# Optimization experiments

Hardware: AMD Instinct MI355X
Metric: run time of the kernel (lower is better)

The kernel has to match this reference:

```python
import jax, jax.numpy as jnp
import numpy as np

DIM = 512
H = 8          # num_heads
C = 64         # dim_head
HID = H * C    # 512
NMEM = H       # num_mem_kv = num_heads


def _rmsnorm_seq(x, w):
    # F.normalize(x, dim=2) * w * sqrt(dim)
    n = jnp.sqrt(jnp.sum(x * x, axis=2, keepdims=True))
    return x / jnp.maximum(n, 1e-12) * w * jnp.asarray(DIM ** 0.5, x.dtype)


def setup_inputs() -> dict:
    key = jax.random.key(0)
    ks = jax.random.split(key, 7)
    b, n = 4, 4096
    x = jax.random.normal(ks[0], (b, n, DIM), dtype=jnp.float32)
    norm_w = jnp.ones((1, 1, DIM), dtype=jnp.float32)
    w_qkv = jax.random.normal(ks[1], (DIM, 3 * HID), dtype=jnp.float32) / np.sqrt(DIM)
    mem_kv = jax.random.normal(ks[2], (2, H, C, NMEM), dtype=jnp.float32)
    w_out = jax.random.normal(ks[3], (HID, DIM), dtype=jnp.float32) / np.sqrt(HID)
    b_out = jax.random.normal(ks[4], (DIM,), dtype=jnp.float32) * 0.01
    out_norm_w = jnp.ones((1, 1, DIM), dtype=jnp.float32)
    return {"x": x, "norm_w": norm_w, "w_qkv": w_qkv, "mem_kv": mem_kv,
            "w_out": w_out, "b_out": b_out, "out_norm_w": out_norm_w}


def reference(x, norm_w, w_qkv, mem_kv, w_out, b_out, out_norm_w):
    b, n, _ = x.shape
    scale = jnp.asarray(C ** -0.5, x.dtype)
    xn = _rmsnorm_seq(x, norm_w)
    qkv = xn @ w_qkv                                   # [b, n, 3*HID]
    q, k, v = jnp.split(qkv, 3, axis=2)
    # b n (h c) -> b h c n
    def to_heads(t):
        return t.reshape(b, n, H, C).transpose(0, 2, 3, 1)
    q, k, v = map(to_heads, (q, k, v))                 # [b, H, C, n]
    mk = jnp.broadcast_to(mem_kv[0], (b, H, C, NMEM))
    mv = jnp.broadcast_to(mem_kv[1], (b, H, C, NMEM))
    k = jnp.concatenate([mk, k], axis=-1)              # [b, H, C, n+NMEM]
    v = jnp.concatenate([mv, v], axis=-1)
    q = jax.nn.softmax(q, axis=-2) * scale             # softmax over feature dim c
    k = jax.nn.softmax(k, axis=-1)                     # softmax over token dim n
    context = jnp.einsum('bhdn,bhen->bhde', k, v)      # [b, H, C, C]
    out = jnp.einsum('bhde,bhdn->bhen', context, q)    # [b, H, C, n]
    out = out.transpose(0, 3, 1, 2).reshape(b, n, HID)  # b h c n -> b n (h c)
    out = out @ w_out + b_out
    return _rmsnorm_seq(out, out_norm_w)
```

## Files before the change

kernel.cpp:

```cpp
#include <hip/hip_runtime.h>
#include <hip/hip_bf16.h>


typedef __attribute__((ext_vector_type(8))) __bf16 bf16x8;
typedef __attribute__((ext_vector_type(4))) __bf16 bf16x4;
typedef __attribute__((ext_vector_type(2))) __bf16 bf16x2;
typedef __attribute__((ext_vector_type(4))) float f32x4;

#define SQRT_DIM 22.627416997969522f

__device__ __forceinline__ void gload_lds16(const void* g, void* l) {
  __builtin_amdgcn_global_load_lds((__attribute__((address_space(1))) void*)g,
                                   (__attribute__((address_space(3))) void*)l, 16, 0, 0);
}

__global__ __launch_bounds__(256) void pre_k(const float* __restrict__ x,
                                             const float* __restrict__ nw,
                                             __bf16* __restrict__ xn,
                                             const float* __restrict__ wqkv,
                                             __bf16* __restrict__ WqkvT) {
  __shared__ float tbuf[64][65];
  const int bid = blockIdx.x;
  const int tid = threadIdx.x;
  if (bid < 4096) {
    const int row = bid * 4 + (tid >> 6);
    const int lane = tid & 63;
    const float4* xr = (const float4*)(x + (size_t)row * 512);
    float4 v0 = xr[lane], v1 = xr[lane + 64];
    float s = v0.x * v0.x + v0.y * v0.y + v0.z * v0.z + v0.w * v0.w +
              v1.x * v1.x + v1.y * v1.y + v1.z * v1.z + v1.w * v1.w;
#pragma unroll
    for (int m = 1; m < 64; m <<= 1) s += __shfl_xor(s, m);
    const float sc = SQRT_DIM / fmaxf(sqrtf(s), 1e-12f);
    const float4* wr4 = (const float4*)nw;
    float4 w0 = wr4[lane], w1 = wr4[lane + 64];
    __bf16* o = xn + (size_t)row * 512;
    bf16x4 a, b2;
    a[0] = (__bf16)(v0.x * sc * w0.x); a[1] = (__bf16)(v0.y * sc * w0.y);
    a[2] = (__bf16)(v0.z * sc * w0.z); a[3] = (__bf16)(v0.w * sc * w0.w);
    b2[0] = (__bf16)(v1.x * sc * w1.x); b2[1] = (__bf16)(v1.y * sc * w1.y);
    b2[2] = (__bf16)(v1.z * sc * w1.z); b2[3] = (__bf16)(v1.w * sc * w1.w);
    *(bf16x4*)(o + lane * 4) = a;
    *(bf16x4*)(o + 256 + lane * 4) = b2;
  } else {
    const int t = bid - 4096;
    const int bx = t % 24, by = t / 24;
    const int n0 = bx * 64, k0 = by * 64;
    const int r = tid >> 4, c4 = (tid & 15) * 4;
#pragma unroll
    for (int p = 0; p < 4; ++p) {
      float4 v = *(const float4*)(wqkv + (size_t)(k0 + p * 16 + r) * 1536 + n0 + c4);
      tbuf[p * 16 + r][c4 + 0] = v.x;
      tbuf[p * 16 + r][c4 + 1] = v.y;
      tbuf[p * 16 + r][c4 + 2] = v.z;
      tbuf[p * 16 + r][c4 + 3] = v.w;
    }
    __syncthreads();
    const int base = (n0 < 512) ? n0
                     : (n0 < 1024 ? 512 + ((n0 - 512) >> 6) * 128
                                  : 512 + ((n0 - 1024) >> 6) * 128 + 64);
#pragma unroll
    for (int p = 0; p < 4; ++p) {
      int c = p * 256 + tid;
      int rn = c >> 4, cc = (c & 15) * 4;
      bf16x4 o;
#pragma unroll
      for (int j = 0; j < 4; ++j) o[j] = (__bf16)tbuf[cc + j][rn];
      *(bf16x4*)(WqkvT + (size_t)(base + rn) * 512 + k0 + cc) = o;
    }
  }
}

__global__ __launch_bounds__(512) void gemm1_k(const __bf16* __restrict__ A,
                                               const __bf16* __restrict__ BT,
                                               __bf16* __restrict__ QS,
                                               __bf16* __restrict__ pctx,
                                               float* __restrict__ pden) {
  __shared__ __align__(16) char smem[65536];
  const int K = 512;
  const int NT = 8;
  const int NX = 12;
  const int tid = threadIdx.x;
  const int lane = tid & 63;
  const int wave = tid >> 6;
  const int wr = (wave >> 1) * 32;
  const int wc = (wave & 1) * 64;
  const int l15 = lane & 15, lg = lane >> 4;
  const int cpx = gridDim.x >> 3;
  const int fid = blockIdx.x;
  const int tile = (fid & 7) * cpx + (fid >> 3);
  const int my = tile / NX;
  const int m0 = my * 128;
  const int n0 = (tile - my * NX) * 128;
  const int sw0 = lg ^ (l15 & 7);
  const int sw1 = (4 + lg) ^ (l15 & 7);

  f32x4 acc[2][4] = {};

  auto stage = [&](int buf, int k0) {
#pragma unroll
    for (int it = 0; it < 2; ++it) {
      int flat = it * 512 + tid;
      int row = flat >> 3;
      int cb = ((flat & 7) ^ (row & 7)) * 16;
      gload_lds16((const char*)(A + (size_t)(m0 + row) * K + k0) + cb,
                  smem + buf * 16384 + flat * 16);
    }
#pragma unroll
    for (int it = 0; it < 2; ++it) {
      int flat = it * 512 + tid;
      int row = flat >> 3;
      int cb = ((flat & 7) ^ (row & 7)) * 16;
      gload_lds16((const char*)(BT + (size_t)(n0 + row) * K + k0) + cb,
                  smem + 32768 + buf * 16384 + flat * 16);
    }
  };

  stage(0, 0);
  stage(1, 64);
  asm volatile("s_waitcnt vmcnt(4)" ::: "memory");
  __builtin_amdgcn_s_barrier();

  for (int kt = 0; kt < NT; ++kt) {
    const int cur = kt & 1;
    const __bf16* Asb = (const __bf16*)(smem + cur * 16384);
    const __bf16* Bsb = (const __bf16*)(smem + 32768 + cur * 16384);
    bf16x8 a0[2], b0[4], a1[2], b1[4];
#pragma unroll
    for (int i = 0; i < 2; ++i) {
      a0[i] = *(const bf16x8*)(&Asb[(wr + i * 16 + l15) * 64 + sw0 * 8]);
      a1[i] = *(const bf16x8*)(&Asb[(wr + i * 16 + l15) * 64 + sw1 * 8]);
    }
#pragma unroll
    for (int i = 0; i < 4; ++i) {
      b0[i] = *(const bf16x8*)(&Bsb[(wc + i * 16 + l15) * 64 + sw0 * 8]);
      b1[i] = *(const bf16x8*)(&Bsb[(wc + i * 16 + l15) * 64 + sw1 * 8]);
    }
    asm volatile("s_waitcnt lgkmcnt(0)" ::: "memory");
    __builtin_amdgcn_sched_barrier(0);
    __builtin_amdgcn_s_barrier();
    if (kt + 2 < NT) stage(cur, (kt + 2) * 64);
    __builtin_amdgcn_s_setprio(1);
#pragma unroll
    for (int mi = 0; mi < 2; ++mi)
#pragma unroll
      for (int ni = 0; ni < 4; ++ni)
        acc[mi][ni] = __builtin_amdgcn_mfma_f32_16x16x32_bf16(a0[mi], b0[ni],
                                                              acc[mi][ni], 0, 0, 0);
    __builtin_amdgcn_s_setprio(0);
    __builtin_amdgcn_s_setprio(1);
#pragma unroll
    for (int mi = 0; mi < 2; ++mi)
#pragma unroll
      for (int ni = 0; ni < 4; ++ni)
        acc[mi][ni] = __builtin_amdgcn_mfma_f32_16x16x32_bf16(a1[mi], b1[ni],
                                                              acc[mi][ni], 0, 0, 0);
    __builtin_amdgcn_s_setprio(0);
    if (kt < NT - 1) {
      if (kt + 2 < NT)
        asm volatile("s_waitcnt vmcnt(4)" ::: "memory");
      else
        asm volatile("s_waitcnt vmcnt(0)" ::: "memory");
      __builtin_amdgcn_s_barrier();
    }
  }

  if (n0 < 512) {
    __bf16* Cs = (__bf16*)smem;
#pragma unroll
    for (int mi = 0; mi < 2; ++mi)
#pragma unroll
      for (int r = 0; r < 4; ++r) {
        float v0_ = acc[mi][0][r], v1_ = acc[mi][1][r], v2_ = acc[mi][2][r],
              v3_ = acc[mi][3][r];
        float mx = fmaxf(fmaxf(v0_, v1_), fmaxf(v2_, v3_));
#pragma unroll
        for (int m = 1; m < 16; m <<= 1) mx = fmaxf(mx, __shfl_xor(mx, m));
        float e0 = __expf(v0_ - mx), e1 = __expf(v1_ - mx),
              e2 = __expf(v2_ - mx), e3 = __expf(v3_ - mx);
        float s = e0 + e1 + e2 + e3;
#pragma unroll
        for (int m = 1; m < 16; m <<= 1) s += __shfl_xor(s, m);
        float inv = 0.125f / s;
        int row = wr + mi * 16 + lg * 4 + r;
        Cs[row * 132 + wc + l15] = (__bf16)(e0 * inv);
        Cs[row * 132 + wc + 16 + l15] = (__bf16)(e1 * inv);
        Cs[row * 132 + wc + 32 + l15] = (__bf16)(e2 * inv);
        Cs[row * 132 + wc + 48 + l15] = (__bf16)(e3 * inv);
      }
    __syncthreads();
    const int sr = tid >> 4, sc = tid & 15;
#pragma unroll
    for (int p = 0; p < 4; ++p) {
      int row = p * 32 + sr;
      bf16x8 v = *(const bf16x8*)(&Cs[row * 132 + sc * 8]);
      *(bf16x8*)(QS + (size_t)(m0 + row) * 512 + n0 + sc * 8) = v;
    }
  } else {
    const int h = (n0 >> 7) - 4;
    __bf16* EKs = (__bf16*)smem;
    __bf16* Vs = (__bf16*)(smem + 16384);
    float* denp = (float*)(smem + 32768);
    float p[4] = {0.0f, 0.0f, 0.0f, 0.0f};
#pragma unroll
    for (int mi = 0; mi < 2; ++mi) {
      const int tok0 = wr + mi * 16 + lg * 4;
#pragma unroll
      for (int ni = 0; ni < 4; ++ni) {
        const int c = ni * 16 + l15;
        bf16x4 pk;
        if (wc == 0) {
#pragma unroll
          for (int r = 0; r < 4; ++r) {
            float e = __expf(acc[mi][ni][r]);
            p[ni] += e;
            pk[r] = (__bf16)e;
          }
          *(bf16x4*)(&EKs[c * 128 + (((tok0 >> 3) ^ (c & 7)) * 8) + (tok0 & 7)]) = pk;
        } else {
#pragma unroll
          for (int r = 0; r < 4; ++r) pk[r] = (__bf16)acc[mi][ni][r];
          *(bf16x4*)(&Vs[c * 128 + (((tok0 >> 3) ^ (c & 7)) * 8) + (tok0 & 7)]) = pk;
        }
      }
    }
    if (wc == 0) {
#pragma unroll
      for (int ni = 0; ni < 4; ++ni) {
        p[ni] += __shfl_xor(p[ni], 16);
        p[ni] += __shfl_xor(p[ni], 32);
      }
      if (lg == 0) {
#pragma unroll
        for (int ni = 0; ni < 4; ++ni)
          denp[(wave >> 1) * 64 + ni * 16 + l15] = p[ni];
      }
    }
    __syncthreads();
    const int b = m0 >> 12, chunk = (m0 & 4095) >> 7;
    const int wg = (b * 8 + h) * 32 + chunk;
    if (tid < 64)
      pden[(size_t)wg * 64 + tid] =
          denp[tid] + denp[64 + tid] + denp[128 + tid] + denp[192 + tid];
    const int dt = wave >> 1;
    const int eb = (wave & 1) * 2;
    f32x4 cacc[2] = {};
#pragma unroll
    for (int kt2 = 0; kt2 < 4; ++kt2) {
      const int d = dt * 16 + l15;
      bf16x8 af = *(const bf16x8*)(&EKs[d * 128 + ((kt2 * 4 + lg) ^ (d & 7)) * 8]);
      bf16x8 bfr[2];
#pragma unroll
      for (int j = 0; j < 2; ++j) {
        int e = (eb + j) * 16 + l15;
        bfr[j] = *(const bf16x8*)(&Vs[e * 128 + ((kt2 * 4 + lg) ^ (e & 7)) * 8]);
      }
#pragma unroll
      for (int j = 0; j < 2; ++j)
        cacc[j] = __builtin_amdgcn_mfma_f32_16x16x32_bf16(af, bfr[j], cacc[j], 0, 0, 0);
    }
    __bf16* op = pctx + (size_t)wg * 4096;
#pragma unroll
    for (int j = 0; j < 2; ++j) {
      int e = (eb + j) * 16 + l15;
#pragma unroll
      for (int r = 0; r < 4; ++r) {
        int d = dt * 16 + lg * 4 + r;
        op[d * 64 + e] = (__bf16)cacc[j][r];
      }
    }
  }
}

__global__ __launch_bounds__(512) void gemm2rms(const __bf16* __restrict__ QS,
                                                const __bf16* __restrict__ W2T,
                                                const float* __restrict__ bias,
                                                const float* __restrict__ onw,
                                                float* __restrict__ out) {
  __shared__ __bf16 As[2][64 * 64];
  __shared__ __bf16 Bs[2][512 * 64];
  __shared__ float rss[64][8];
  const int K = 512;
  const int NT = 8;
  const int tid = threadIdx.x;
  const int lane = tid & 63;
  const int wave = tid >> 6;
  const int wc = wave * 64;
  const int l15 = lane & 15, lg = lane >> 4;
  const int cpx = gridDim.x >> 3;
  const int fid = blockIdx.x;
  const int tile = (fid & 7) * cpx + (fid >> 3);
  const int m0 = tile * 64;
  const __bf16* bt = W2T + (size_t)(m0 >> 12) * 262144;

  f32x4 acc[4][4] = {};

  auto stage = [&](int buf, int k0) {
    {
      int flat = tid;
      int row = flat >> 3;
      int cb = ((flat & 7) ^ (row & 7)) * 16;
      gload_lds16((const char*)(QS + (size_t)(m0 + row) * K + k0) + cb,
                  (char*)(&As[buf][0]) + flat * 16);
    }
#pragma unroll
    for (int it = 0; it < 8; ++it) {
      int flat = it * 512 + tid;
      int row = flat >> 3;
      int cb = ((flat & 7) ^ (row & 7)) * 16;
      gload_lds16((const char*)(bt + (size_t)row * K + k0) + cb,
                  (char*)(&Bs[buf][0]) + flat * 16);
    }
  };

  stage(0, 0);
  stage(1, 64);
  asm volatile("s_waitcnt vmcnt(9)" ::: "memory");
  __builtin_amdgcn_s_barrier();

  for (int kt = 0; kt < NT; ++kt) {
    const int cur = kt & 1;
    bf16x8 a0[4], b0[4], a1[4], b1[4];
    const int sw0 = lg ^ (l15 & 7);
    const int sw1 = (4 + lg) ^ (l15 & 7);
#pragma unroll
    for (int i = 0; i < 4; ++i) {
      a0[i] = *(const bf16x8*)(&As[cur][(i * 16 + l15) * 64 + sw0 * 8]);
      b0[i] = *(const bf16x8*)(&Bs[cur][(wc + i * 16 + l15) * 64 + sw0 * 8]);
      a1[i] = *(const bf16x8*)(&As[cur][(i * 16 + l15) * 64 + sw1 * 8]);
      b1[i] = *(const bf16x8*)(&Bs[cur][(wc + i * 16 + l15) * 64 + sw1 * 8]);
    }
    asm volatile("s_waitcnt lgkmcnt(0)" ::: "memory");
    __builtin_amdgcn_sched_barrier(0);
    __builtin_amdgcn_s_barrier();
    if (kt + 2 < NT) stage(cur, (kt + 2) * 64);
    __builtin_amdgcn_s_setprio(1);
#pragma unroll
    for (int mi = 0; mi < 4; ++mi)
#pragma unroll
      for (int ni = 0; ni < 4; ++ni)
        acc[mi][ni] = __builtin_amdgcn_mfma_f32_16x16x32_bf16(a0[mi], b0[ni],
                                                              acc[mi][ni], 0, 0, 0);
    __builtin_amdgcn_s_setprio(0);
    __builtin_amdgcn_s_setprio(1);
#pragma unroll
    for (int mi = 0; mi < 4; ++mi)
#pragma unroll
      for (int ni = 0; ni < 4; ++ni)
        acc[mi][ni] = __builtin_amdgcn_mfma_f32_16x16x32_bf16(a1[mi], b1[ni],
                                                              acc[mi][ni], 0, 0, 0);
    __builtin_amdgcn_s_setprio(0);
    if (kt < NT - 1) {
      if (kt + 2 < NT)
        asm volatile("s_waitcnt vmcnt(9)" ::: "memory");
      else
        asm volatile("s_waitcnt vmcnt(0)" ::: "memory");
      __builtin_amdgcn_s_barrier();
    }
  }

  float bv[4], wv[4];
#pragma unroll
  for (int ni = 0; ni < 4; ++ni) {
    int col = wc + ni * 16 + l15;
    bv[ni] = bias[col];
    wv[ni] = onw[col];
  }
  float vv[4][4][4];
#pragma unroll
  for (int mi = 0; mi < 4; ++mi)
#pragma unroll
    for (int ni = 0; ni < 4; ++ni)
#pragma unroll
      for (int r = 0; r < 4; ++r) vv[mi][ni][r] = acc[mi][ni][r] + bv[ni];
#pragma unroll
  for (int mi = 0; mi < 4; ++mi)
#pragma unroll
    for (int r = 0; r < 4; ++r) {
      float ps = vv[mi][0][r] * vv[mi][0][r] + vv[mi][1][r] * vv[mi][1][r] +
                 vv[mi][2][r] * vv[mi][2][r] + vv[mi][3][r] * vv[mi][3][r];
#pragma unroll
      for (int m = 1; m < 16; m <<= 1) ps += __shfl_xor(ps, m);
      if (l15 == 0) rss[mi * 16 + lg * 4 + r][wave] = ps;
    }
  __syncthreads();
#pragma unroll
  for (int mi = 0; mi < 4; ++mi)
#pragma unroll
    for (int r = 0; r < 4; ++r) {
      int row = mi * 16 + lg * 4 + r;
      float ss = rss[row][0] + rss[row][1] + rss[row][2] + rss[row][3] +
                 rss[row][4] + rss[row][5] + rss[row][6] + rss[row][7];
      float sc = SQRT_DIM / fmaxf(sqrtf(ss), 1e-12f);
      size_t rb = (size_t)(m0 + row) * 512;
#pragma unroll
      for (int ni = 0; ni < 4; ++ni)
        out[rb + wc + ni * 16 + l15] = vv[mi][ni][r] * sc * wv[ni];
    }
}

__global__ __launch_bounds__(256) void ctx_final(const __bf16* __restrict__ pctx,
                                                 const float* __restrict__ pden,
                                                 const float* __restrict__ memkv,
                                                 float* __restrict__ ctx) {
  const int bh = blockIdx.x >> 3, dg = blockIdx.x & 7;
  const int h = bh & 7;
  const int tid = threadIdx.x;
  __shared__ float sden[8][9];
  if (tid < 64) {
    const int dl = tid >> 3, part = tid & 7;
    const int d = dg * 8 + dl;
    float s = 0.0f;
#pragma unroll
    for (int c = 0; c < 4; ++c)
      s += pden[((size_t)bh * 32 + part * 4 + c) * 64 + d];
    if (part == 0) {
#pragma unroll
      for (int m = 0; m < 8; ++m)
        s += __expf(memkv[(size_t)h * 512 + d * 8 + m]);
    }
    sden[dl][part] = s;
  }
  __syncthreads();
  const int dl = tid >> 5, e2 = (tid & 31) * 2;
  const int d = dg * 8 + dl;
  float den = sden[dl][0] + sden[dl][1] + sden[dl][2] + sden[dl][3] +
              sden[dl][4] + sden[dl][5] + sden[dl][6] + sden[dl][7];
  float invd = 1.0f / den;
  float s0 = 0.0f, s1 = 0.0f;
#pragma unroll
  for (int m = 0; m < 8; ++m) {
    float ek = __expf(memkv[(size_t)h * 512 + d * 8 + m]);
    s0 += ek * memkv[4096 + (size_t)h * 512 + e2 * 8 + m];
    s1 += ek * memkv[4096 + (size_t)h * 512 + (e2 + 1) * 8 + m];
  }
#pragma unroll
  for (int c = 0; c < 32; ++c) {
    bf16x2 p = *(const bf16x2*)(pctx + ((size_t)bh * 32 + c) * 4096 + d * 64 + e2);
    s0 += (float)p[0];
    s1 += (float)p[1];
  }
  float2 o = make_float2(s0 * invd, s1 * invd);
  *(float2*)(ctx + (size_t)bh * 4096 + d * 64 + e2) = o;
}

__global__ __launch_bounds__(256) void make_w2t(const float* __restrict__ ctx,
                                                const float* __restrict__ wout,
                                                __bf16* __restrict__ W2T) {
  const int wg = blockIdx.x;
  const int b = wg >> 6, h = (wg >> 3) & 7, jc = wg & 7;
  const int j0 = jc * 64;
  const int tid = threadIdx.x;
  __shared__ float cs[64][65];
  __shared__ float wo[64][64];
  const float* ch = ctx + ((size_t)b * 8 + h) * 4096;
#pragma unroll
  for (int it = 0; it < 16; ++it) {
    int flat = it * 256 + tid;
    cs[flat >> 6][flat & 63] = ch[flat];
  }
#pragma unroll
  for (int it = 0; it < 16; ++it) {
    int flat = it * 256 + tid;
    int e = flat >> 6, j = flat & 63;
    wo[e][j] = wout[(size_t)(h * 64 + e) * 512 + j0 + j];
  }
  __syncthreads();
  const int d = tid & 63;
  const int jg = (tid >> 6) * 16;
  for (int jj = 0; jj < 16; ++jj) {
    int j = jg + jj;
    float s = 0.0f;
#pragma unroll
    for (int e = 0; e < 64; ++e) s += cs[d][e] * wo[e][j];
    W2T[(size_t)b * 262144 + (size_t)(j0 + j) * 512 + h * 64 + d] = (__bf16)s;
  }
}

extern "C" void kernel_launch(void* const* d_in, const int* in_sizes, int n_in,
                              void* d_out, int out_size, void* d_ws, size_t ws_size,
                              hipStream_t stream) {
  const float* x = (const float*)d_in[0];
  const float* norm_w = (const float*)d_in[1];
  const float* w_qkv = (const float*)d_in[2];
  const float* mem_kv = (const float*)d_in[3];
  const float* w_out = (const float*)d_in[4];
  const float* b_out = (const float*)d_in[5];
  const float* onw = (const float*)d_in[6];

  char* ws = (char*)d_ws;
  __bf16* xn = (__bf16*)(ws + 0);
  __bf16* WqkvT = (__bf16*)(ws + 16777216);
  __bf16* pctx = (__bf16*)(ws + 18350080);
  __bf16* QS = (__bf16*)(ws + 51904512);
  float* pden = (float*)(ws + 68681728);
  float* ctx = (float*)(ws + 68943872);
  __bf16* W2T = (__bf16*)(ws + 69468160);

  pre_k<<<4288, 256, 0, stream>>>(x, norm_w, xn, w_qkv, WqkvT);
  gemm1_k<<<1536, 512, 0, stream>>>(xn, WqkvT, QS, pctx, pden);
  ctx_final<<<256, 256, 0, stream>>>(pctx, pden, mem_kv, ctx);
  make_w2t<<<256, 256, 0, stream>>>(ctx, w_out, W2T);
  gemm2rms<<<256, 512, 0, stream>>>(QS, W2T, b_out, onw, (float*)d_out);
}
```

Before: 86.03 us.

## Load GEMM2 operands directly from global memory instead of LDS double-buffering

Removes the LDS staging buffers, async global-to-LDS copies, waitcnts and barriers from the output projection GEMM. Each wave now loads its A and B fragments straight from global memory into registers, with the k loop fully unrolled. This drops the LDS footprint (which may raise occupancy) and the synchronisation overhead. The cost is that the A tile is no longer shared across the 8 waves, so each wave re-reads it from global/L2, and there is no explicit prefetch pipelining.

```diff
diff --git a/kernel.cpp b/kernel.cpp
--- a/kernel.cpp
+++ b/kernel.cpp
@@ -277,11 +277,7 @@
                                                 const float* __restrict__ bias,
                                                 const float* __restrict__ onw,
                                                 float* __restrict__ out) {
-  __shared__ __bf16 As[2][64 * 64];
-  __shared__ __bf16 Bs[2][512 * 64];
   __shared__ float rss[64][8];
-  const int K = 512;
-  const int NT = 8;
   const int tid = threadIdx.x;
   const int lane = tid & 63;
   const int wave = tid >> 6;
@@ -294,69 +290,31 @@
   const __bf16* bt = W2T + (size_t)(m0 >> 12) * 262144;
 
   f32x4 acc[4][4] = {};
-
-  auto stage = [&](int buf, int k0) {
-    {
-      int flat = tid;
-      int row = flat >> 3;
-      int cb = ((flat & 7) ^ (row & 7)) * 16;
-      gload_lds16((const char*)(QS + (size_t)(m0 + row) * K + k0) + cb,
-                  (char*)(&As[buf][0]) + flat * 16);
-    }
-#pragma unroll
-    for (int it = 0; it < 8; ++it) {
-      int flat = it * 512 + tid;
-      int row = flat >> 3;
-      int cb = ((flat & 7) ^ (row & 7)) * 16;
-      gload_lds16((const char*)(bt + (size_t)row * K + k0) + cb,
-                  (char*)(&Bs[buf][0]) + flat * 16);
-    }
-  };
-
-  stage(0, 0);
-  stage(1, 64);
-  asm volatile("s_waitcnt vmcnt(9)" ::: "memory");
-  __builtin_amdgcn_s_barrier();
-
-  for (int kt = 0; kt < NT; ++kt) {
-    const int cur = kt & 1;
-    bf16x8 a0[4], b0[4], a1[4], b1[4];
-    const int sw0 = lg ^ (l15 & 7);
-    const int sw1 = (4 + lg) ^ (l15 & 7);
+  const __bf16* aRow0 = QS + (size_t)(m0 + l15) * 512 + lg * 8;
+  const __bf16* bRow0 = bt + (size_t)(wc + l15) * 512 + lg * 8;
+
+#pragma unroll
+  for (int kt = 0; kt < 8; ++kt) {
+    bf16x8 a0[4], a1[4], b0[4], b1[4];
 #pragma unroll
     for (int i = 0; i < 4; ++i) {
-      a0[i] = *(const bf16x8*)(&As[cur][(i * 16 + l15) * 64 + sw0 * 8]);
-      b0[i] = *(const bf16x8*)(&Bs[cur][(wc + i * 16 + l15) * 64 + sw0 * 8]);
-      a1[i] = *(const bf16x8*)(&As[cur][(i * 16 + l15) * 64 + sw1 * 8]);
-      b1[i] = *(const bf16x8*)(&Bs[cur][(wc + i * 16 + l15) * 64 + sw1 * 8]);
-    }
-    asm volatile("s_waitcnt lgkmcnt(0)" ::: "memory");
-    __builtin_amdgcn_sched_barrier(0);
-    __builtin_amdgcn_s_barrier();
-    if (kt + 2 < NT) stage(cur, (kt + 2) * 64);
-    __builtin_amdgcn_s_setprio(1);
+      a0[i] = *(const bf16x8*)(aRow0 + (size_t)i * 16 * 512 + kt * 64);
+      a1[i] = *(const bf16x8*)(aRow0 + (size_t)i * 16 * 512 + kt * 64 + 32);
+      b0[i] = *(const bf16x8*)(bRow0 + (size_t)i * 16 * 512 + kt * 64);
+      b1[i] = *(const bf16x8*)(bRow0 + (size_t)i * 16 * 512 + kt * 64 + 32);
+    }
 #pragma unroll
     for (int mi = 0; mi < 4; ++mi)
 #pragma unroll
       for (int ni = 0; ni < 4; ++ni)
         acc[mi][ni] = __builtin_amdgcn_mfma_f32_16x16x32_bf16(a0[mi], b0[ni],
                                                               acc[mi][ni], 0, 0, 0);
-    __builtin_amdgcn_s_setprio(0);
-    __builtin_amdgcn_s_setprio(1);
 #pragma unroll
     for (int mi = 0; mi < 4; ++mi)
 #pragma unroll
       for (int ni = 0; ni < 4; ++ni)
         acc[mi][ni] = __builtin_amdgcn_mfma_f32_16x16x32_bf16(a1[mi], b1[ni],
                                                               acc[mi][ni], 0, 0, 0);
-    __builtin_amdgcn_s_setprio(0);
-    if (kt < NT - 1) {
-      if (kt + 2 < NT)
-        asm volatile("s_waitcnt vmcnt(9)" ::: "memory");
-      else
-        asm volatile("s_waitcnt vmcnt(0)" ::: "memory");
-      __builtin_amdgcn_s_barrier();
-    }
   }
 
   float bv[4], wv[4];
```

After: 105.2 us. 1.22x slower.

## Restructure gemm1 K-loop into 4-stage pipeline of 32-wide K slices

Applied to the files above, without the earlier changes.

Replaces the double-buffered K loop (64-wide tiles, 8 iterations) in gemm1_k with a four-deep ring of 32-wide K slices (16 iterations), using a new XOR swizzle suited to 64-byte rows. The aim is to keep more global-to-LDS loads in flight so load latency is hidden better in this short K=512 GEMM. In exchange it doubles the number of barriers and waitcnt points per tile and halves the MFMA work between them. A few variables were renamed to avoid name clashes.

```diff
diff --git a/kernel.cpp b/kernel.cpp
--- a/kernel.cpp
+++ b/kernel.cpp
@@ -78,7 +78,7 @@
                                                float* __restrict__ pden) {
   __shared__ __align__(16) char smem[65536];
   const int K = 512;
-  const int NT = 8;
+  const int NH = 16;
   const int NX = 12;
   const int tid = threadIdx.x;
   const int lane = tid & 63;
@@ -92,75 +92,54 @@
   const int my = tile / NX;
   const int m0 = my * 128;
   const int n0 = (tile - my * NX) * 128;
-  const int sw0 = lg ^ (l15 & 7);
-  const int sw1 = (4 + lg) ^ (l15 & 7);
 
   f32x4 acc[2][4] = {};
 
-  auto stage = [&](int buf, int k0) {
-#pragma unroll
-    for (int it = 0; it < 2; ++it) {
-      int flat = it * 512 + tid;
-      int row = flat >> 3;
-      int cb = ((flat & 7) ^ (row & 7)) * 16;
-      gload_lds16((const char*)(A + (size_t)(m0 + row) * K + k0) + cb,
-                  smem + buf * 16384 + flat * 16);
-    }
-#pragma unroll
-    for (int it = 0; it < 2; ++it) {
-      int flat = it * 512 + tid;
-      int row = flat >> 3;
-      int cb = ((flat & 7) ^ (row & 7)) * 16;
-      gload_lds16((const char*)(BT + (size_t)(n0 + row) * K + k0) + cb,
-                  smem + 32768 + buf * 16384 + flat * 16);
-    }
+  auto stage = [&](int q, int h) {
+    const int row = tid >> 2, c = tid & 3;
+    const int sc = c ^ (row & 3) ^ ((row >> 2) & 3);
+    gload_lds16((const char*)(A + (size_t)(m0 + row) * K + h * 32) + sc * 16,
+                smem + q * 8192 + tid * 16);
+    gload_lds16((const char*)(BT + (size_t)(n0 + row) * K + h * 32) + sc * 16,
+                smem + 32768 + q * 8192 + tid * 16);
   };
 
   stage(0, 0);
-  stage(1, 64);
-  asm volatile("s_waitcnt vmcnt(4)" ::: "memory");
+  stage(1, 1);
+  stage(2, 2);
+  stage(3, 3);
+  asm volatile("s_waitcnt vmcnt(6)" ::: "memory");
   __builtin_amdgcn_s_barrier();
 
-  for (int kt = 0; kt < NT; ++kt) {
-    const int cur = kt & 1;
-    const __bf16* Asb = (const __bf16*)(smem + cur * 16384);
-    const __bf16* Bsb = (const __bf16*)(smem + 32768 + cur * 16384);
-    bf16x8 a0[2], b0[4], a1[2], b1[4];
+  for (int h = 0; h < NH; ++h) {
+    const int q = h & 3;
+    const __bf16* Aq = (const __bf16*)(smem + q * 8192);
+    const __bf16* Bq = (const __bf16*)(smem + 32768 + q * 8192);
+    bf16x8 af[2], bfr[4];
 #pragma unroll
     for (int i = 0; i < 2; ++i) {
-      a0[i] = *(const bf16x8*)(&Asb[(wr + i * 16 + l15) * 64 + sw0 * 8]);
-      a1[i] = *(const bf16x8*)(&Asb[(wr + i * 16 + l15) * 64 + sw1 * 8]);
+      int r = wr + i * 16 + l15;
+      af[i] = *(const bf16x8*)(&Aq[r * 32 + (lg ^ (r & 3) ^ ((r >> 2) & 3)) * 8]);
     }
 #pragma unroll
     for (int i = 0; i < 4; ++i) {
-      b0[i] = *(const bf16x8*)(&Bsb[(wc + i * 16 + l15) * 64 + sw0 * 8]);
-      b1[i] = *(const bf16x8*)(&Bsb[(wc + i * 16 + l15) * 64 + sw1 * 8]);
+      int r = wc + i * 16 + l15;
+      bfr[i] = *(const bf16x8*)(&Bq[r * 32 + (lg ^ (r & 3) ^ ((r >> 2) & 3)) * 8]);
     }
     asm volatile("s_waitcnt lgkmcnt(0)" ::: "memory");
     __builtin_amdgcn_sched_barrier(0);
     __builtin_amdgcn_s_barrier();
-    if (kt + 2 < NT) stage(cur, (kt + 2) * 64);
+    if (h + 4 < NH) stage(q, h + 4);
     __builtin_amdgcn_s_setprio(1);
 #pragma unroll
     for (int mi = 0; mi < 2; ++mi)
 #pragma unroll
       for (int ni = 0; ni < 4; ++ni)
-        acc[mi][ni] = __builtin_amdgcn_mfma_f32_16x16x32_bf16(a0[mi], b0[ni],
+        acc[mi][ni] = __builtin_amdgcn_mfma_f32_16x16x32_bf16(af[mi], bfr[ni],
                                                               acc[mi][ni], 0, 0, 0);
     __builtin_amdgcn_s_setprio(0);
-    __builtin_amdgcn_s_setprio(1);
-#pragma unroll
-    for (int mi = 0; mi < 2; ++mi)
-#pragma unroll
-      for (int ni = 0; ni < 4; ++ni)
-        acc[mi][ni] = __builtin_amdgcn_mfma_f32_16x16x32_bf16(a1[mi], b1[ni],
-                                                              acc[mi][ni], 0, 0, 0);
-    __builtin_amdgcn_s_setprio(0);
-    if (kt < NT - 1) {
-      if (kt + 2 < NT)
-        asm volatile("s_waitcnt vmcnt(4)" ::: "memory");
-      else
-        asm volatile("s_waitcnt vmcnt(0)" ::: "memory");
+    if (h < NH - 1) {
+      asm volatile("s_waitcnt vmcnt(6)" ::: "memory");
       __builtin_amdgcn_s_barrier();
     }
   }
@@ -189,12 +168,12 @@
         Cs[row * 132 + wc + 48 + l15] = (__bf16)(e3 * inv);
       }
     __syncthreads();
-    const int sr = tid >> 4, sc = tid & 15;
+    const int sr = tid >> 4, sc2 = tid & 15;
 #pragma unroll
     for (int p = 0; p < 4; ++p) {
       int row = p * 32 + sr;
-      bf16x8 v = *(const bf16x8*)(&Cs[row * 132 + sc * 8]);
-      *(bf16x8*)(QS + (size_t)(m0 + row) * 512 + n0 + sc * 8) = v;
+      bf16x8 v = *(const bf16x8*)(&Cs[row * 132 + sc2 * 8]);
+      *(bf16x8*)(QS + (size_t)(m0 + row) * 512 + n0 + sc2 * 8) = v;
     }
   } else {
     const int h = (n0 >> 7) - 4;
@@ -248,16 +227,16 @@
 #pragma unroll
     for (int kt2 = 0; kt2 < 4; ++kt2) {
       const int d = dt * 16 + l15;
-      bf16x8 af = *(const bf16x8*)(&EKs[d * 128 + ((kt2 * 4 + lg) ^ (d & 7)) * 8]);
-      bf16x8 bfr[2];
+      bf16x8 af2 = *(const bf16x8*)(&EKs[d * 128 + ((kt2 * 4 + lg) ^ (d & 7)) * 8]);
+      bf16x8 bfr2[2];
 #pragma unroll
       for (int j = 0; j < 2; ++j) {
         int e = (eb + j) * 16 + l15;
-        bfr[j] = *(const bf16x8*)(&Vs[e * 128 + ((kt2 * 4 + lg) ^ (e & 7)) * 8]);
+        bfr2[j] = *(const bf16x8*)(&Vs[e * 128 + ((kt2 * 4 + lg) ^ (e & 7)) * 8]);
       }
 #pragma unroll
       for (int j = 0; j < 2; ++j)
-        cacc[j] = __builtin_amdgcn_mfma_f32_16x16x32_bf16(af, bfr[j], cacc[j], 0, 0, 0);
+        cacc[j] = __builtin_amdgcn_mfma_f32_16x16x32_bf16(af2, bfr2[j], cacc[j], 0, 0, 0);
     }
     __bf16* op = pctx + (size_t)wg * 4096;
 #pragma unroll
```

After: 86.73 us. About the same (+0.8%).
